# Performance work log

Measured on AMD Instinct MI355X. Metric: run time of the kernel, lower is better.

The kernel has to match this reference:

```python
import jax, jax.numpy as jnp
import numpy as np

N_NODES = 50000
N_EDGES = 400000
D = 512
L = 3


def setup_inputs() -> dict:
    key = jax.random.key(0)
    ks = jax.random.split(key, 6)
    x = jax.random.normal(ks[0], (N_NODES, D), dtype=jnp.float32)
    edge_index = jax.random.randint(ks[1], (2, N_EDGES), 0, N_NODES, dtype=jnp.int64)
    edge_weight = jax.random.uniform(ks[2], (N_EDGES,), dtype=jnp.float32)
    Wl = jax.random.normal(ks[3], (L, D, D), dtype=jnp.float32) / np.sqrt(D)
    Wr = jax.random.normal(ks[4], (L, D, D), dtype=jnp.float32) / np.sqrt(D)
    b = jnp.zeros((L, D), dtype=jnp.float32)
    return {"x": x, "edge_index": edge_index, "edge_weight": edge_weight,
            "Wl": Wl, "Wr": Wr, "b": b}


def reference(x, edge_index, edge_weight, Wl, Wr, b):
    # PyG SAGEConv (mean aggregation, root weight, bias on lin_l):
    #   out_i = W_l @ mean_{j in N(i)} (w_ji * x_j) + b + W_r @ x_i
    # edge_index[0] = source j, edge_index[1] = destination i.
    src, dst = edge_index[0], edge_index[1]
    # in-degree for mean normalization (count of incoming edges per node)
    deg = jax.ops.segment_sum(jnp.ones_like(edge_weight), dst, num_segments=N_NODES)
    inv_deg = jnp.where(deg > 0, 1.0 / deg, 0.0)[:, None]  # [N,1]
    z = x
    for i in range(L):
        msg = z[src] * edge_weight[:, None]                       # [E, D] gather
        agg = jax.ops.segment_sum(msg, dst, num_segments=N_NODES) * inv_deg  # [N, D]
        z = jax.nn.relu(agg @ Wl[i] + b[i] + z @ Wr[i])           # [N, D]
    return z
```

## Files before the change

### kernel.cpp

```cpp
#include <hip/hip_runtime.h>

#define NN 50000
#define NE 400000
#define DD 512
#define MT 391
#define SB 49

typedef unsigned short ushort_t;
typedef __attribute__((ext_vector_type(8))) short bf16x8;
typedef __attribute__((ext_vector_type(8))) unsigned short u16x8;
typedef __attribute__((ext_vector_type(4))) float f32x4;

#define GLD16(g, l) __builtin_amdgcn_global_load_lds( \
    (const __attribute__((address_space(1))) void*)(g), \
    (__attribute__((address_space(3))) void*)(l), 16, 0, 0)

__device__ __forceinline__ float bf2f(unsigned short u) {
    union { unsigned u; float f; } c; c.u = ((unsigned)u) << 16; return c.f;
}
__device__ __forceinline__ unsigned short f2bf(float f) {
    union { float f; unsigned u; } c; c.f = f;
    unsigned r = c.u + 0x7FFFu + ((c.u >> 16) & 1u);
    return (unsigned short)(r >> 16);
}
__device__ __forceinline__ void split2(float v, unsigned short& h, unsigned short& l) {
    h = f2bf(v);
    l = f2bf(v - bf2f(h));
}


__global__ void hist_kernel(const int* __restrict__ dst, int* __restrict__ deg) {
    int e = blockIdx.x * blockDim.x + threadIdx.x;
    if (e < NE) atomicAdd(&deg[dst[e]], 1);
}

__global__ __launch_bounds__(1024) void scan_local(const int* __restrict__ deg,
                                                   int* __restrict__ offs,
                                                   int* __restrict__ bsum) {
    __shared__ int sdata[1024];
    int i = blockIdx.x * 1024 + threadIdx.x;
    int v = (i < NN) ? deg[i] : 0;
    sdata[threadIdx.x] = v;
    __syncthreads();
    for (int off = 1; off < 1024; off <<= 1) {
        int add = (threadIdx.x >= off) ? sdata[threadIdx.x - off] : 0;
        __syncthreads();
        sdata[threadIdx.x] += add;
        __syncthreads();
    }
    if (i < NN) offs[i] = sdata[threadIdx.x] - v;
    if (threadIdx.x == 1023) bsum[blockIdx.x] = sdata[1023];
}

__global__ void scan_carry(int* __restrict__ bsum) {
    int lane = threadIdx.x;
    int orig = (lane < SB) ? bsum[lane] : 0;
    int v = orig;
    #pragma unroll
    for (int off = 1; off < 64; off <<= 1) {
        int n = __shfl_up(v, off, 64);
        if (lane >= off) v += n;
    }
    if (lane < SB) bsum[lane] = v - orig;
}

__global__ __launch_bounds__(1024) void scan_apply(const int* __restrict__ deg,
                                                   const int* __restrict__ bsum,
                                                   int* __restrict__ offs,
                                                   float* __restrict__ inv_deg) {
    int i = blockIdx.x * 1024 + threadIdx.x;
    if (i < NN) {
        offs[i] += bsum[blockIdx.x];
        int d = deg[i];
        inv_deg[i] = (d > 0) ? (1.0f / (float)d) : 0.0f;
    }
    if (i == 0) offs[NN] = NE;
}

__global__ void scatter_kernel(const int* __restrict__ src, const int* __restrict__ dst,
                               const float* __restrict__ w, const int* __restrict__ offsets,
                               int* __restrict__ cursor, int2* __restrict__ esw) {
    int e = blockIdx.x * blockDim.x + threadIdx.x;
    if (e < NE) {
        int d = dst[e];
        int pos = offsets[d] + atomicAdd(&cursor[d], 1);
        esw[pos] = make_int2(src[e], __float_as_int(w[e]));
    }
}


__global__ void convert_x_kernel(const float* __restrict__ x, ushort_t* __restrict__ xh) {
    const int total = NN * DD / 8;
    for (int i = blockIdx.x * blockDim.x + threadIdx.x; i < total; i += gridDim.x * blockDim.x) {
        float4 v1 = ((const float4*)x)[2 * i];
        float4 v2 = ((const float4*)x)[2 * i + 1];
        u16x8 o;
        o[0] = f2bf(v1.x); o[1] = f2bf(v1.y); o[2] = f2bf(v1.z); o[3] = f2bf(v1.w);
        o[4] = f2bf(v2.x); o[5] = f2bf(v2.y); o[6] = f2bf(v2.z); o[7] = f2bf(v2.w);
        ((u16x8*)xh)[i] = o;
    }
}

__global__ void split_wt_kernel(const float* __restrict__ Wl, const float* __restrict__ Wr,
                                ushort_t* __restrict__ wt) {
    __shared__ float tile[32][33];
    int mat = blockIdx.z;
    int layer = mat >> 1;
    const float* W = (mat & 1) ? (Wr + (size_t)layer * DD * DD) : (Wl + (size_t)layer * DD * DD);
    ushort_t* oh = wt + ((size_t)layer * 4 + (size_t)(mat & 1) * 2) * DD * DD;
    ushort_t* ol = oh + (size_t)DD * DD;
    int k0 = blockIdx.y * 32, n0 = blockIdx.x * 32;
    #pragma unroll
    for (int r = 0; r < 4; ++r)
        tile[threadIdx.y * 4 + r][threadIdx.x] =
            W[(size_t)(k0 + threadIdx.y * 4 + r) * DD + n0 + threadIdx.x];
    __syncthreads();
    #pragma unroll
    for (int r = 0; r < 4; ++r) {
        int n = n0 + threadIdx.y * 4 + r, k = k0 + threadIdx.x;
        unsigned short h, l;
        split2(tile[threadIdx.x][threadIdx.y * 4 + r], h, l);
        oh[(size_t)n * DD + k] = h;
        ol[(size_t)n * DD + k] = l;
    }
}


__global__ __launch_bounds__(256) void aggregate_kernel(
        const ushort_t* __restrict__ zh, const int2* __restrict__ esw,
        const int* __restrict__ offsets, const float* __restrict__ inv_deg,
        ushort_t* __restrict__ aggh) {
    int node = blockIdx.x * 4 + (threadIdx.x >> 6);
    if (node >= NN) return;
    int lane = threadIdx.x & 63;
    const ushort_t* zbase = zh + lane * 8;
    int s0 = offsets[node], s1 = offsets[node + 1];
    float a[8] = {0.f, 0.f, 0.f, 0.f, 0.f, 0.f, 0.f, 0.f};
    int e = s0;
    for (; e + 4 <= s1; e += 4) {
        int2 p0 = esw[e], p1 = esw[e + 1], p2 = esw[e + 2], p3 = esw[e + 3];
        u16x8 v0 = *(const u16x8*)(zbase + (size_t)p0.x * DD);
        u16x8 v1 = *(const u16x8*)(zbase + (size_t)p1.x * DD);
        u16x8 v2 = *(const u16x8*)(zbase + (size_t)p2.x * DD);
        u16x8 v3 = *(const u16x8*)(zbase + (size_t)p3.x * DD);
        float w0 = __int_as_float(p0.y), w1 = __int_as_float(p1.y);
        float w2 = __int_as_float(p2.y), w3 = __int_as_float(p3.y);
        #pragma unroll
        for (int j = 0; j < 8; ++j) {
            a[j] = fmaf(w0, bf2f(v0[j]), a[j]);
            a[j] = fmaf(w1, bf2f(v1[j]), a[j]);
            a[j] = fmaf(w2, bf2f(v2[j]), a[j]);
            a[j] = fmaf(w3, bf2f(v3[j]), a[j]);
        }
    }
    for (; e < s1; ++e) {
        int2 p = esw[e];
        u16x8 v = *(const u16x8*)(zbase + (size_t)p.x * DD);
        float w = __int_as_float(p.y);
        #pragma unroll
        for (int j = 0; j < 8; ++j) a[j] = fmaf(w, bf2f(v[j]), a[j]);
    }
    float inv = inv_deg[node];
    u16x8 o;
    #pragma unroll
    for (int j = 0; j < 8; ++j) o[j] = f2bf(a[j] * inv);
    *(u16x8*)&aggh[(size_t)node * DD + lane * 8] = o;
}


template<bool FINAL>
__global__ __launch_bounds__(256) void gemm_mfma(
        const ushort_t* __restrict__ aggh, const ushort_t* __restrict__ zh,
        const ushort_t* __restrict__ wt,
        const float* __restrict__ bias,
        ushort_t* __restrict__ outh, float* __restrict__ outf) {
    __shared__ char smem[49152];
    const int AT = 0, BH = 16384, BL = 32768;

    const int tid = threadIdx.x;
    const int lane = tid & 63;
    const int w = tid >> 6;
    const int wr = w >> 1, wc = w & 1;

    const int orig = blockIdx.y * gridDim.x + blockIdx.x;
    const int q = 195, r = 4;
    const int xcd = orig & 7, kpos = orig >> 3;
    const int wg = (xcd < r ? xcd * (q + 1) : r * (q + 1) + (xcd - r) * q) + kpos;
    const int m0 = (wg >> 2) * 128;
    const int n0 = (wg & 3) * 128;

    const int rsub = lane >> 3;
    const int sl = (lane & 7) ^ rsub;
    int offA[4], offB[4];
    #pragma unroll
    for (int j = 0; j < 4; ++j) {
        int qq = w * 4 + j;
        int ra = m0 + qq * 8 + rsub;
        if (ra >= NN) ra = NN - 1;
        offA[j] = ra * DD + sl * 8;
        int rb = n0 + qq * 8 + rsub;
        offB[j] = rb * DD + sl * 8;
    }

    const int rlo = lane & 15;
    const int khi = lane >> 4;
    const int sw7 = rlo & 7;
    int aRow[4], bRow[4];
    #pragma unroll
    for (int i = 0; i < 4; ++i) {
        aRow[i] = (wr * 64 + i * 16 + rlo) * 128;
        bRow[i] = (wc * 64 + i * 16 + rlo) * 128;
    }

    f32x4 acc[4][4];
    #pragma unroll
    for (int mi = 0; mi < 4; ++mi)
        #pragma unroll
        for (int ni = 0; ni < 4; ++ni)
            acc[mi][ni] = f32x4{0.f, 0.f, 0.f, 0.f};

    #pragma unroll
    for (int pass = 0; pass < 2; ++pass) {
        const ushort_t* A  = pass ? zh : aggh;
        const ushort_t* Bh = wt + (size_t)(pass ? 2 : 0) * DD * DD;
        const ushort_t* Bl = Bh + (size_t)DD * DD;
        for (int k0 = 0; k0 < DD; k0 += 64) {
            #pragma unroll
            for (int j = 0; j < 4; ++j) {
                int qo = (w * 4 + j) * 1024;
                GLD16(A + offA[j] + k0, smem + AT + qo);
                GLD16(Bh + offB[j] + k0, smem + BH + qo);
                GLD16(Bl + offB[j] + k0, smem + BL + qo);
            }
            __syncthreads();
            #pragma unroll
            for (int kk = 0; kk < 2; ++kk) {
                const int pa = ((kk * 4 + khi) ^ sw7) * 16;
                bf16x8 a_f[4], b_h[4], b_l[4];
                #pragma unroll
                for (int i = 0; i < 4; ++i) {
                    a_f[i] = *(const bf16x8*)(smem + AT + aRow[i] + pa);
                    b_h[i] = *(const bf16x8*)(smem + BH + bRow[i] + pa);
                    b_l[i] = *(const bf16x8*)(smem + BL + bRow[i] + pa);
                }
                #pragma unroll
                for (int mi = 0; mi < 4; ++mi)
                    #pragma unroll
                    for (int ni = 0; ni < 4; ++ni) {
                        acc[mi][ni] = __builtin_amdgcn_mfma_f32_16x16x32_bf16(
                            a_f[mi], b_h[ni], acc[mi][ni], 0, 0, 0);
                        acc[mi][ni] = __builtin_amdgcn_mfma_f32_16x16x32_bf16(
                            a_f[mi], b_l[ni], acc[mi][ni], 0, 0, 0);
                    }
            }
            __syncthreads();
        }
    }

    float bv[4];
    #pragma unroll
    for (int ni = 0; ni < 4; ++ni)
        bv[ni] = bias[n0 + wc * 64 + ni * 16 + rlo];
    #pragma unroll
    for (int mi = 0; mi < 4; ++mi) {
        #pragma unroll
        for (int j = 0; j < 4; ++j) {
            int row = m0 + wr * 64 + mi * 16 + khi * 4 + j;
            if (row < NN) {
                #pragma unroll
                for (int ni = 0; ni < 4; ++ni) {
                    int col = n0 + wc * 64 + ni * 16 + rlo;
                    float v = acc[mi][ni][j] + bv[ni];
                    v = v > 0.f ? v : 0.f;
                    if (FINAL) outf[(size_t)row * DD + col] = v;
                    else       outh[(size_t)row * DD + col] = f2bf(v);
                }
            }
        }
    }
}

extern "C" void kernel_launch(void* const* d_in, const int* in_sizes, int n_in,
                              void* d_out, int out_size, void* d_ws, size_t ws_size,
                              hipStream_t stream) {
    const float* x  = (const float*)d_in[0];
    const int*   ei = (const int*)d_in[1];
    const float* ew = (const float*)d_in[2];
    const float* Wl = (const float*)d_in[3];
    const float* Wr = (const float*)d_in[4];
    const float* b  = (const float*)d_in[5];
    float* out = (float*)d_out;

    const int* srcIdx = ei;
    const int* dstIdx = ei + NE;

    const size_t ND = (size_t)NN * DD;
    char* p = (char*)d_ws;
    ushort_t* zA   = (ushort_t*)p; p += ND * 2;
    ushort_t* zB   = (ushort_t*)p; p += ND * 2;
    ushort_t* aggA = (ushort_t*)p; p += ND * 2;
    ushort_t* wt   = (ushort_t*)p; p += (size_t)12 * DD * DD * 2;
    int* deg      = (int*)p; p += sizeof(int) * NN;
    int* cursor   = (int*)p; p += sizeof(int) * NN;
    int2* esw     = (int2*)p; p += sizeof(int2) * NE;
    float* invdeg = (float*)p; p += sizeof(float) * NN;
    int* offsets  = (int*)p; p += sizeof(int) * (NN + 1);
    int* bsum     = (int*)p; p += sizeof(int) * 64;

    hipMemsetAsync(deg, 0, sizeof(int) * 2 * NN, stream);
    hist_kernel<<<(NE + 255) / 256, 256, 0, stream>>>(dstIdx, deg);
    scan_local<<<SB, 1024, 0, stream>>>(deg, offsets, bsum);
    scan_carry<<<1, 64, 0, stream>>>(bsum);
    scan_apply<<<SB, 1024, 0, stream>>>(deg, bsum, offsets, invdeg);
    scatter_kernel<<<(NE + 255) / 256, 256, 0, stream>>>(srcIdx, dstIdx, ew, offsets,
                                                          cursor, esw);
    convert_x_kernel<<<2048, 256, 0, stream>>>(x, zA);
    split_wt_kernel<<<dim3(16, 16, 6), dim3(32, 8), 0, stream>>>(Wl, Wr, wt);

    dim3 ggrid(4, MT);
    dim3 agrid((NN + 3) / 4);
    const size_t WTL = (size_t)4 * DD * DD;

    aggregate_kernel<<<agrid, 256, 0, stream>>>(zA, esw, offsets, invdeg, aggA);
    gemm_mfma<false><<<ggrid, 256, 0, stream>>>(aggA, zA, wt, b, zB, nullptr);
    aggregate_kernel<<<agrid, 256, 0, stream>>>(zB, esw, offsets, invdeg, aggA);
    gemm_mfma<false><<<ggrid, 256, 0, stream>>>(aggA, zB, wt + WTL, b + DD, zA, nullptr);
    aggregate_kernel<<<agrid, 256, 0, stream>>>(zA, esw, offsets, invdeg, aggA);
    gemm_mfma<true><<<ggrid, 256, 0, stream>>>(aggA, zA, wt + 2 * WTL, b + 2 * DD,
                                               nullptr, out);
}
```

Before: 749.4 us.

## Use single bf16 weights in GEMM and wave-broadcast edge lists in aggregation

Drops the hi/lo bf16 split of the weight matrices, so each GEMM issues half as many MFMAs, loads half as much weight data into LDS and uses less shared memory. The aggregation kernel now loads up to 64 edge records per wave in one coalesced read and broadcasts them with shuffles, instead of each lane reading every record separately. The cost is lower weight precision (plain bf16 rounding of W), which could push results outside tolerance.

Measured after the change: 622.7 us. -16.9%, faster.

```diff
diff --git a/kernel.cpp b/kernel.cpp
--- a/kernel.cpp
+++ b/kernel.cpp
@@ -22,10 +22,6 @@
     union { float f; unsigned u; } c; c.f = f;
     unsigned r = c.u + 0x7FFFu + ((c.u >> 16) & 1u);
     return (unsigned short)(r >> 16);
-}
-__device__ __forceinline__ void split2(float v, unsigned short& h, unsigned short& l) {
-    h = f2bf(v);
-    l = f2bf(v - bf2f(h));
 }
 
 
@@ -101,14 +97,13 @@
     }
 }
 
-__global__ void split_wt_kernel(const float* __restrict__ Wl, const float* __restrict__ Wr,
-                                ushort_t* __restrict__ wt) {
+__global__ void convert_wt_kernel(const float* __restrict__ Wl, const float* __restrict__ Wr,
+                                  ushort_t* __restrict__ wt) {
     __shared__ float tile[32][33];
     int mat = blockIdx.z;
     int layer = mat >> 1;
     const float* W = (mat & 1) ? (Wr + (size_t)layer * DD * DD) : (Wl + (size_t)layer * DD * DD);
-    ushort_t* oh = wt + ((size_t)layer * 4 + (size_t)(mat & 1) * 2) * DD * DD;
-    ushort_t* ol = oh + (size_t)DD * DD;
+    ushort_t* oh = wt + ((size_t)layer * 2 + (size_t)(mat & 1)) * DD * DD;
     int k0 = blockIdx.y * 32, n0 = blockIdx.x * 32;
     #pragma unroll
     for (int r = 0; r < 4; ++r)
@@ -118,10 +113,7 @@
     #pragma unroll
     for (int r = 0; r < 4; ++r) {
         int n = n0 + threadIdx.y * 4 + r, k = k0 + threadIdx.x;
-        unsigned short h, l;
-        split2(tile[threadIdx.x][threadIdx.y * 4 + r], h, l);
-        oh[(size_t)n * DD + k] = h;
-        ol[(size_t)n * DD + k] = l;
+        oh[(size_t)n * DD + k] = f2bf(tile[threadIdx.x][threadIdx.y * 4 + r]);
     }
 }
 
@@ -136,29 +128,18 @@
     const ushort_t* zbase = zh + lane * 8;
     int s0 = offsets[node], s1 = offsets[node + 1];
     float a[8] = {0.f, 0.f, 0.f, 0.f, 0.f, 0.f, 0.f, 0.f};
-    int e = s0;
-    for (; e + 4 <= s1; e += 4) {
-        int2 p0 = esw[e], p1 = esw[e + 1], p2 = esw[e + 2], p3 = esw[e + 3];
-        u16x8 v0 = *(const u16x8*)(zbase + (size_t)p0.x * DD);
-        u16x8 v1 = *(const u16x8*)(zbase + (size_t)p1.x * DD);
-        u16x8 v2 = *(const u16x8*)(zbase + (size_t)p2.x * DD);
-        u16x8 v3 = *(const u16x8*)(zbase + (size_t)p3.x * DD);
-        float w0 = __int_as_float(p0.y), w1 = __int_as_float(p1.y);
-        float w2 = __int_as_float(p2.y), w3 = __int_as_float(p3.y);
-        #pragma unroll
-        for (int j = 0; j < 8; ++j) {
-            a[j] = fmaf(w0, bf2f(v0[j]), a[j]);
-            a[j] = fmaf(w1, bf2f(v1[j]), a[j]);
-            a[j] = fmaf(w2, bf2f(v2[j]), a[j]);
-            a[j] = fmaf(w3, bf2f(v3[j]), a[j]);
+    for (int base = s0; base < s1; base += 64) {
+        int cnt = s1 - base; if (cnt > 64) cnt = 64;
+        int2 p = make_int2(0, 0);
+        if (base + lane < s1) p = esw[base + lane];
+        #pragma unroll 4
+        for (int j = 0; j < cnt; ++j) {
+            int   s = __shfl(p.x, j);
+            float w = __int_as_float(__shfl(p.y, j));
+            u16x8 v = *(const u16x8*)(zbase + (size_t)s * DD);
+            #pragma unroll
+            for (int q = 0; q < 8; ++q) a[q] = fmaf(w, bf2f(v[q]), a[q]);
         }
-    }
-    for (; e < s1; ++e) {
-        int2 p = esw[e];
-        u16x8 v = *(const u16x8*)(zbase + (size_t)p.x * DD);
-        float w = __int_as_float(p.y);
-        #pragma unroll
-        for (int j = 0; j < 8; ++j) a[j] = fmaf(w, bf2f(v[j]), a[j]);
     }
     float inv = inv_deg[node];
     u16x8 o;
@@ -174,8 +155,8 @@
         const ushort_t* __restrict__ wt,
         const float* __restrict__ bias,
         ushort_t* __restrict__ outh, float* __restrict__ outf) {
-    __shared__ char smem[49152];
-    const int AT = 0, BH = 16384, BL = 32768;
+    __shared__ char smem[32768];
+    const int AT = 0, BT = 16384;
 
     const int tid = threadIdx.x;
     const int lane = tid & 63;
@@ -221,37 +202,31 @@
 
     #pragma unroll
     for (int pass = 0; pass < 2; ++pass) {
-        const ushort_t* A  = pass ? zh : aggh;
-        const ushort_t* Bh = wt + (size_t)(pass ? 2 : 0) * DD * DD;
-        const ushort_t* Bl = Bh + (size_t)DD * DD;
+        const ushort_t* A = pass ? zh : aggh;
+        const ushort_t* B = wt + (size_t)pass * DD * DD;
         for (int k0 = 0; k0 < DD; k0 += 64) {
             #pragma unroll
             for (int j = 0; j < 4; ++j) {
                 int qo = (w * 4 + j) * 1024;
                 GLD16(A + offA[j] + k0, smem + AT + qo);
-                GLD16(Bh + offB[j] + k0, smem + BH + qo);
-                GLD16(Bl + offB[j] + k0, smem + BL + qo);
+                GLD16(B + offB[j] + k0, smem + BT + qo);
             }
             __syncthreads();
             #pragma unroll
             for (int kk = 0; kk < 2; ++kk) {
                 const int pa = ((kk * 4 + khi) ^ sw7) * 16;
-                bf16x8 a_f[4], b_h[4], b_l[4];
+                bf16x8 a_f[4], b_f[4];
                 #pragma unroll
                 for (int i = 0; i < 4; ++i) {
                     a_f[i] = *(const bf16x8*)(smem + AT + aRow[i] + pa);
-                    b_h[i] = *(const bf16x8*)(smem + BH + bRow[i] + pa);
-                    b_l[i] = *(const bf16x8*)(smem + BL + bRow[i] + pa);
+                    b_f[i] = *(const bf16x8*)(smem + BT + bRow[i] + pa);
                 }
                 #pragma unroll
                 for (int mi = 0; mi < 4; ++mi)
                     #pragma unroll
-                    for (int ni = 0; ni < 4; ++ni) {
+                    for (int ni = 0; ni < 4; ++ni)
                         acc[mi][ni] = __builtin_amdgcn_mfma_f32_16x16x32_bf16(
-                            a_f[mi], b_h[ni], acc[mi][ni], 0, 0, 0);
-                        acc[mi][ni] = __builtin_amdgcn_mfma_f32_16x16x32_bf16(
-                            a_f[mi], b_l[ni], acc[mi][ni], 0, 0, 0);
-                    }
+                            a_f[mi], b_f[ni], acc[mi][ni], 0, 0, 0);
             }
             __syncthreads();
         }
@@ -299,7 +274,7 @@
     ushort_t* zA   = (ushort_t*)p; p += ND * 2;
     ushort_t* zB   = (ushort_t*)p; p += ND * 2;
     ushort_t* aggA = (ushort_t*)p; p += ND * 2;
-    ushort_t* wt   = (ushort_t*)p; p += (size_t)12 * DD * DD * 2;
+    ushort_t* wt   = (ushort_t*)p; p += (size_t)6 * DD * DD * 2;
     int* deg      = (int*)p; p += sizeof(int) * NN;
     int* cursor   = (int*)p; p += sizeof(int) * NN;
     int2* esw     = (int2*)p; p += sizeof(int2) * NE;
@@ -315,11 +290,11 @@
     scatter_kernel<<<(NE + 255) / 256, 256, 0, stream>>>(srcIdx, dstIdx, ew, offsets,
                                                           cursor, esw);
     convert_x_kernel<<<2048, 256, 0, stream>>>(x, zA);
-    split_wt_kernel<<<dim3(16, 16, 6), dim3(32, 8), 0, stream>>>(Wl, Wr, wt);
+    convert_wt_kernel<<<dim3(16, 16, 6), dim3(32, 8), 0, stream>>>(Wl, Wr, wt);
 
     dim3 ggrid(4, MT);
     dim3 agrid((NN + 3) / 4);
-    const size_t WTL = (size_t)4 * DD * DD;
+    const size_t WTL = (size_t)2 * DD * DD;
 
     aggregate_kernel<<<agrid, 256, 0, stream>>>(zA, esw, offsets, invdeg, aggA);
     gemm_mfma<false><<<ggrid, 256, 0, stream>>>(aggA, zA, wt, b, zB, nullptr);
```
